# Kernel optimization log

Measured on AMD Instinct MI355X. Metric: run time of the kernel, lower is better.

The kernel has to match this reference:

```python
import jax, jax.numpy as jnp
import numpy as np


def setup_inputs() -> dict:
    key = jax.random.key(0)
    k1, k2, k3, k4, k5, k6 = jax.random.split(key, 6)
    B, T, U, D, V = 4, 512, 128, 512, 512
    speech = jax.random.normal(k1, (B, T, D), dtype=jnp.float32)
    text = jax.random.normal(k2, (B, U, D), dtype=jnp.float32)
    W = jax.random.normal(k3, (V, D), dtype=jnp.float32) / np.sqrt(D)
    b = jax.random.normal(k4, (V,), dtype=jnp.float32) * 0.01
    speech_len = jax.random.randint(k5, (B,), 1, T + 1, dtype=jnp.int32)
    text_len = jax.random.randint(k6, (B,), 1, U + 1, dtype=jnp.int32)
    return {"speech": speech, "text": text, "W": W, "b": b,
            "speech_len": speech_len, "text_len": text_len}


def reference(speech, text, W, b, speech_len, text_len):
    # RNN-T joint network: broadcast-add encoder and predictor outputs,
    # then project to vocab. speech: [B,T,D], text: [B,U,D].
    joint = speech[:, :, None, :] + text[:, None, :, :]       # [B,T,U,D]
    logits = jnp.einsum('btud,vd->btuv', joint, W) + b         # [B,T,U,V]
    return logits, speech_len, text_len
```

## Files before the change

kernel.cpp:

```cpp
#include <hip/hip_runtime.h>

#define B_ 4
#define T_ 512
#define U_ 128
#define D_ 512
#define V_ 512
#define MS (B_ * T_)
#define MT (B_ * U_)
#define MTOT (MS + MT)
#define LOGITS_ELEMS ((size_t)B_ * T_ * U_ * V_)

#define TM 128
#define TN 64
#define TK 32
#define NTILES (D_ / TK)
#define XSTR 132
#define WSTR 68

typedef float f32x4 __attribute__((ext_vector_type(4)));

__global__ __launch_bounds__(256, 2) void gemm_joint(
    const float* __restrict__ speech, const float* __restrict__ text,
    const float* __restrict__ W, const float* __restrict__ bias,
    float* __restrict__ S, float* __restrict__ Tx)
{
    __shared__ float Xt[TK][XSTR];
    __shared__ float Wt[TK][WSTR];

    const int tid = threadIdx.x;
    const int m0 = blockIdx.x * TM;
    const int n0 = blockIdx.y * TN;
    const int tx = tid & 15;
    const int ty = tid >> 4;

    const float* xbase = (m0 < MS) ? (speech + (size_t)m0 * D_)
                                   : (text + (size_t)(m0 - MS) * D_);

    float acc[8][4] = {};
    float4 xr[4], wr[2];

    #pragma unroll
    for (int i = 0; i < 4; ++i) {
        const int q = tid + 256 * i;
        xr[i] = *(const float4*)(xbase + (size_t)(q >> 3) * D_ + ((q & 7) << 2));
    }
    #pragma unroll
    for (int i = 0; i < 2; ++i) {
        const int q = tid + 256 * i;
        wr[i] = *(const float4*)(W + (size_t)(n0 + (q >> 3)) * D_ + ((q & 7) << 2));
    }
    #pragma unroll
    for (int i = 0; i < 4; ++i) {
        const int q = tid + 256 * i;
        const int r = q >> 3, c = (q & 7) << 2;
        Xt[c + 0][r] = xr[i].x; Xt[c + 1][r] = xr[i].y;
        Xt[c + 2][r] = xr[i].z; Xt[c + 3][r] = xr[i].w;
    }
    #pragma unroll
    for (int i = 0; i < 2; ++i) {
        const int q = tid + 256 * i;
        const int r = q >> 3, c = (q & 7) << 2;
        Wt[c + 0][r] = wr[i].x; Wt[c + 1][r] = wr[i].y;
        Wt[c + 2][r] = wr[i].z; Wt[c + 3][r] = wr[i].w;
    }
    __syncthreads();

    for (int t = 0; t < NTILES; ++t) {
        if (t + 1 < NTILES) {
            const int kn = (t + 1) * TK;
            #pragma unroll
            for (int i = 0; i < 4; ++i) {
                const int q = tid + 256 * i;
                xr[i] = *(const float4*)(xbase + (size_t)(q >> 3) * D_ + kn + ((q & 7) << 2));
            }
            #pragma unroll
            for (int i = 0; i < 2; ++i) {
                const int q = tid + 256 * i;
                wr[i] = *(const float4*)(W + (size_t)(n0 + (q >> 3)) * D_ + kn + ((q & 7) << 2));
            }
        }

        #pragma unroll 8
        for (int k = 0; k < TK; ++k) {
            const float4 a0 = *(const float4*)&Xt[k][ty * 8];
            const float4 a1 = *(const float4*)&Xt[k][ty * 8 + 4];
            const float4 b0 = *(const float4*)&Wt[k][tx * 4];
            const float av[8] = {a0.x, a0.y, a0.z, a0.w, a1.x, a1.y, a1.z, a1.w};
            const float bv[4] = {b0.x, b0.y, b0.z, b0.w};
            #pragma unroll
            for (int i = 0; i < 8; ++i)
                #pragma unroll
                for (int j = 0; j < 4; ++j)
                    acc[i][j] += av[i] * bv[j];
        }

        if (t + 1 < NTILES) {
            __syncthreads();
            #pragma unroll
            for (int i = 0; i < 4; ++i) {
                const int q = tid + 256 * i;
                const int r = q >> 3, c = (q & 7) << 2;
                Xt[c + 0][r] = xr[i].x; Xt[c + 1][r] = xr[i].y;
                Xt[c + 2][r] = xr[i].z; Xt[c + 3][r] = xr[i].w;
            }
            #pragma unroll
            for (int i = 0; i < 2; ++i) {
                const int q = tid + 256 * i;
                const int r = q >> 3, c = (q & 7) << 2;
                Wt[c + 0][r] = wr[i].x; Wt[c + 1][r] = wr[i].y;
                Wt[c + 2][r] = wr[i].z; Wt[c + 3][r] = wr[i].w;
            }
            __syncthreads();
        }
    }

    const int vbase = n0 + tx * 4;
    #pragma unroll
    for (int i = 0; i < 8; ++i) {
        const int m = m0 + ty * 8 + i;
        float4 o;
        o.x = acc[i][0]; o.y = acc[i][1]; o.z = acc[i][2]; o.w = acc[i][3];
        if (m < MS) {
            *(float4*)(S + (size_t)m * V_ + vbase) = o;
        } else {
            o.x += bias[vbase + 0];
            o.y += bias[vbase + 1];
            o.z += bias[vbase + 2];
            o.w += bias[vbase + 3];
            *(float4*)(Tx + (size_t)(m - MS) * V_ + vbase) = o;
        }
    }
}

__global__ __launch_bounds__(256, 8) void bcast_add(
    const float* __restrict__ S, const float* __restrict__ Tx,
    const int* __restrict__ sl, const int* __restrict__ tl,
    float* __restrict__ out)
{
    const int V4 = V_ / 4;
    const int bt = blockIdx.x;
    const int b  = bt >> 9;
    const int tid = threadIdx.x;

    if (bt == 0 && tid < 2 * B_) {
        out[LOGITS_ELEMS + tid] = (tid < B_) ? (float)sl[tid]
                                             : (float)tl[tid - B_];
    }

    const f32x4* S4 = (const f32x4*)S + (size_t)bt * V4;
    const f32x4* T4 = (const f32x4*)Tx + (size_t)b * U_ * V4;
    f32x4* O4 = (f32x4*)out + (size_t)bt * U_ * V4;

    const f32x4 sv = S4[tid & (V4 - 1)];

    #pragma unroll 8
    for (int idx = tid; idx < U_ * V4; idx += 256) {
        const f32x4 tv = T4[idx];
        __builtin_nontemporal_store(sv + tv, &O4[idx]);
    }
}

extern "C" void kernel_launch(void* const* d_in, const int* in_sizes, int n_in,
                              void* d_out, int out_size, void* d_ws, size_t ws_size,
                              hipStream_t stream) {
    const float* speech = (const float*)d_in[0];
    const float* text   = (const float*)d_in[1];
    const float* W      = (const float*)d_in[2];
    const float* bias   = (const float*)d_in[3];
    const int*   sl     = (const int*)d_in[4];
    const int*   tl     = (const int*)d_in[5];
    float* out = (float*)d_out;

    float* S  = (float*)d_ws;
    float* Tx = S + (size_t)MS * V_;

    dim3 g1(MTOT / TM, V_ / TN);
    gemm_joint<<<g1, 256, 0, stream>>>(speech, text, W, bias, S, Tx);

    bcast_add<<<MS, 256, 0, stream>>>(S, Tx, sl, tl, out);
}
```

Measured before the change: 573.8 us.

## Split the K dimension of the projection GEMM across two partial buffers

The projection GEMM is launched with a z dimension of two, and each half reduces over half of D into separate workspace partials. The broadcast-add kernel sums the two partials while forming the logits, and the bias is applied only by the first half. This doubles the number of GEMM blocks to fill more compute units. In exchange it adds extra partial-sum reads in the bandwidth-bound broadcast loop, and it only applies when the workspace is large enough.

```diff
diff --git a/kernel.cpp b/kernel.cpp
--- a/kernel.cpp
+++ b/kernel.cpp
@@ -13,16 +13,19 @@
 #define TM 128
 #define TN 64
 #define TK 32
-#define NTILES (D_ / TK)
 #define XSTR 132
 #define WSTR 68
+
+#define S_ELEMS ((size_t)MS * V_)
+#define TX_ELEMS ((size_t)MT * V_)
+#define PSTRIDE (S_ELEMS + TX_ELEMS)
 
 typedef float f32x4 __attribute__((ext_vector_type(4)));
 
 __global__ __launch_bounds__(256, 2) void gemm_joint(
     const float* __restrict__ speech, const float* __restrict__ text,
     const float* __restrict__ W, const float* __restrict__ bias,
-    float* __restrict__ S, float* __restrict__ Tx)
+    float* __restrict__ S, float* __restrict__ Tx, int ktiles)
 {
     __shared__ float Xt[TK][XSTR];
     __shared__ float Wt[TK][WSTR];
@@ -30,9 +33,14 @@
     const int tid = threadIdx.x;
     const int m0 = blockIdx.x * TM;
     const int n0 = blockIdx.y * TN;
+    const int z  = blockIdx.z;
+    const int kbase = z * ktiles * TK;
     const int tx = tid & 15;
     const int ty = tid >> 4;
 
+    S  += (size_t)z * PSTRIDE;
+    Tx += (size_t)z * PSTRIDE;
+
     const float* xbase = (m0 < MS) ? (speech + (size_t)m0 * D_)
                                    : (text + (size_t)(m0 - MS) * D_);
 
@@ -42,12 +50,12 @@
     #pragma unroll
     for (int i = 0; i < 4; ++i) {
         const int q = tid + 256 * i;
-        xr[i] = *(const float4*)(xbase + (size_t)(q >> 3) * D_ + ((q & 7) << 2));
+        xr[i] = *(const float4*)(xbase + (size_t)(q >> 3) * D_ + kbase + ((q & 7) << 2));
     }
     #pragma unroll
     for (int i = 0; i < 2; ++i) {
         const int q = tid + 256 * i;
-        wr[i] = *(const float4*)(W + (size_t)(n0 + (q >> 3)) * D_ + ((q & 7) << 2));
+        wr[i] = *(const float4*)(W + (size_t)(n0 + (q >> 3)) * D_ + kbase + ((q & 7) << 2));
     }
     #pragma unroll
     for (int i = 0; i < 4; ++i) {
@@ -65,9 +73,9 @@
     }
     __syncthreads();
 
-    for (int t = 0; t < NTILES; ++t) {
-        if (t + 1 < NTILES) {
-            const int kn = (t + 1) * TK;
+    for (int t = 0; t < ktiles; ++t) {
+        if (t + 1 < ktiles) {
+            const int kn = kbase + (t + 1) * TK;
             #pragma unroll
             for (int i = 0; i < 4; ++i) {
                 const int q = tid + 256 * i;
@@ -94,7 +102,7 @@
                     acc[i][j] += av[i] * bv[j];
         }
 
-        if (t + 1 < NTILES) {
+        if (t + 1 < ktiles) {
             __syncthreads();
             #pragma unroll
             for (int i = 0; i < 4; ++i) {
@@ -123,15 +131,18 @@
         if (m < MS) {
             *(float4*)(S + (size_t)m * V_ + vbase) = o;
         } else {
-            o.x += bias[vbase + 0];
-            o.y += bias[vbase + 1];
-            o.z += bias[vbase + 2];
-            o.w += bias[vbase + 3];
+            if (kbase == 0) {
+                o.x += bias[vbase + 0];
+                o.y += bias[vbase + 1];
+                o.z += bias[vbase + 2];
+                o.w += bias[vbase + 3];
+            }
             *(float4*)(Tx + (size_t)(m - MS) * V_ + vbase) = o;
         }
     }
 }
 
+template <bool SPLIT>
 __global__ __launch_bounds__(256, 8) void bcast_add(
     const float* __restrict__ S, const float* __restrict__ Tx,
     const int* __restrict__ sl, const int* __restrict__ tl,
@@ -151,11 +162,13 @@
     const f32x4* T4 = (const f32x4*)Tx + (size_t)b * U_ * V4;
     f32x4* O4 = (f32x4*)out + (size_t)bt * U_ * V4;
 
-    const f32x4 sv = S4[tid & (V4 - 1)];
+    f32x4 sv = S4[tid & (V4 - 1)];
+    if (SPLIT) sv += S4[(PSTRIDE / 4) + (tid & (V4 - 1))];
 
     #pragma unroll 8
     for (int idx = tid; idx < U_ * V4; idx += 256) {
-        const f32x4 tv = T4[idx];
+        f32x4 tv = T4[idx];
+        if (SPLIT) tv += T4[(PSTRIDE / 4) + idx];
         __builtin_nontemporal_store(sv + tv, &O4[idx]);
     }
 }
@@ -172,10 +185,17 @@
     float* out = (float*)d_out;
 
     float* S  = (float*)d_ws;
-    float* Tx = S + (size_t)MS * V_;
-
-    dim3 g1(MTOT / TM, V_ / TN);
-    gemm_joint<<<g1, 256, 0, stream>>>(speech, text, W, bias, S, Tx);
-
-    bcast_add<<<MS, 256, 0, stream>>>(S, Tx, sl, tl, out);
+    float* Tx = S + S_ELEMS;
+
+    const bool split = ws_size >= 2 * PSTRIDE * sizeof(float);
+
+    if (split) {
+        dim3 g1(MTOT / TM, V_ / TN, 2);
+        gemm_joint<<<g1, 256, 0, stream>>>(speech, text, W, bias, S, Tx, (D_ / TK) / 2);
+        bcast_add<true><<<MS, 256, 0, stream>>>(S, Tx, sl, tl, out);
+    } else {
+        dim3 g1(MTOT / TM, V_ / TN, 1);
+        gemm_joint<<<g1, 256, 0, stream>>>(speech, text, W, bias, S, Tx, D_ / TK);
+        bcast_add<false><<<MS, 256, 0, stream>>>(S, Tx, sl, tl, out);
+    }
 }
```

After: 561.0 us. -2.2%, faster.
